# Performance work log

Hardware: AMD Instinct MI355X
Metric: run time of the kernel (lower is better)

Reference implementation:

```python
import jax, jax.numpy as jnp
import numpy as np

D = 20          # embedding dim (hardcoded in original module)
N_REL = 200     # relation vocab size (table has N_REL+1 rows)
N_TIME = 365    # time embedding table size
L = 3           # propagation layers
E = 2_000_000   # edges per layer
N = 1_000_000   # node-slot pool per layer
B = 64          # batch size
N_ENT = 1_000_003


def setup_inputs() -> dict:
    key = jax.random.key(0)
    ks = jax.random.split(key, 16)
    src_idx = jax.random.randint(ks[0], (L, E), 0, N, dtype=jnp.int32)
    dst_idx = jax.random.randint(ks[1], (L, E), 0, N, dtype=jnp.int32)
    rel_idx = jax.random.randint(ks[2], (L, E), 0, N_REL + 1, dtype=jnp.int32)
    qrel_idx = jax.random.randint(ks[3], (L, E), 0, N_REL + 1, dtype=jnp.int32)
    # signed relative time (edge_time - query_time); abs() must stay < N_TIME
    rel_time = jax.random.randint(ks[4], (L, E), -(N_TIME - 1), N_TIME, dtype=jnp.int32)
    node_batch = jax.random.randint(ks[5], (N,), 0, B, dtype=jnp.int32)
    node_ent = jnp.arange(N, dtype=jnp.int32)  # unique entity per final node slot
    s = 0.1
    rela_embed = jax.random.normal(ks[6], (N_REL + 1, D), jnp.float32) * s
    time_embed = jax.random.normal(ks[7], (N_TIME, D), jnp.float32) * s
    w_att1 = jax.random.normal(ks[8], (30, 3 * D), jnp.float32) * s
    w_att2 = jax.random.normal(ks[9], (1, 30), jnp.float32) * s
    w_past = jax.random.normal(ks[10], (D, D), jnp.float32) * s
    w_now = jax.random.normal(ks[11], (D, D), jnp.float32) * s
    w_future = jax.random.normal(ks[12], (D, D), jnp.float32) * s
    w_cls = jax.random.normal(ks[13], (D,), jnp.float32) * s
    b_cls = jnp.zeros((), jnp.float32)
    return dict(src_idx=src_idx, dst_idx=dst_idx, rel_idx=rel_idx,
                qrel_idx=qrel_idx, rel_time=rel_time, node_batch=node_batch,
                node_ent=node_ent, rela_embed=rela_embed, time_embed=time_embed,
                w_att1=w_att1, w_att2=w_att2, w_past=w_past, w_now=w_now,
                w_future=w_future, w_cls=w_cls, b_cls=b_cls,
                batch_size=B, n_ent=N_ENT)


def reference(src_idx, dst_idx, rel_idx, qrel_idx, rel_time, node_batch,
              node_ent, rela_embed, time_embed, w_att1, w_att2, w_past,
              w_now, w_future, w_cls, b_cls, batch_size, n_ent):
    n_layers = src_idx.shape[0]
    n_nodes = node_batch.shape[0]
    d = rela_embed.shape[1]
    hidden = jnp.zeros((n_nodes, d), dtype=rela_embed.dtype)
    for l in range(n_layers):
        rt = rel_time[l]                         # [E] signed relative time
        h_src = hidden[src_idx[l]]               # [E, D] gather
        r_emb = rela_embed[rel_idx[l]]           # [E, D]
        t_emb = time_embed[jnp.abs(rt)]          # [E, D]
        embed_rel = h_src + r_emb + t_emb
        # conditional time-branch MLP (mask-partitioned linear, same math as
        # the original's boolean-masked assignments)
        fut = embed_rel @ w_future.T
        now = embed_rel @ w_now.T
        pst = embed_rel @ w_past.T
        transformed = jnp.where((rt > 0)[:, None], fut,
                       jnp.where((rt == 0)[:, None], now, pst))
        # attention over concat(hidden_src, rel_emb, query_rel_emb)  [E, 3D]
        att_in = jnp.concatenate([h_src, r_emb, rela_embed[qrel_idx[l]]], axis=1)
        score = jax.nn.sigmoid(jax.nn.relu(att_in @ w_att1.T) @ w_att2.T)  # [E,1]
        msg = score * transformed                # [E, D]
        hidden = jax.ops.segment_sum(msg, dst_idx[l], num_segments=n_nodes)
        hidden = jax.nn.leaky_relu(hidden)       # default slope 0.01, as torch
    result = hidden @ w_cls + b_cls              # [N]
    score_all = jnp.zeros((batch_size, n_ent), dtype=result.dtype)
    score_all = score_all.at[node_batch, node_ent].set(result)
    return score_all
```

## Files before the change

### kernel.cpp

```cpp
#include <hip/hip_runtime.h>
#include <hip/hip_bf16.h>
#include <cstdint>

#define DD 20
#define HID 30
#define NB_SCAN 1024
#define MROW 21

__device__ __forceinline__ void load20(const float* __restrict__ p, float* r){
  const float4* q = (const float4*)p;
#pragma unroll
  for (int i=0;i<5;i++){ float4 v=q[i]; r[4*i+0]=v.x; r[4*i+1]=v.y; r[4*i+2]=v.z; r[4*i+3]=v.w; }
}

__global__ void k_prep(const float* __restrict__ rela, const float* __restrict__ w1,
                       const float* __restrict__ wp, const float* __restrict__ wn,
                       const float* __restrict__ wf,
                       float* __restrict__ W3, float* __restrict__ AR, float* __restrict__ AQ,
                       int nrel){
  int t = blockIdx.x*blockDim.x + threadIdx.x;
  if (t < 3*DD*DD){
    int s = t/(DD*DD), idx = t%(DD*DD);
    W3[t] = (s==0)?wp[idx]:((s==1)?wn[idx]:wf[idx]);
  }
  if (t < nrel*HID){
    int r=t/HID, j=t-r*HID;
    float sr=0.f, sq=0.f;
#pragma unroll
    for (int k=0;k<DD;k++){
      float e = rela[r*DD+k];
      sr += e*w1[j*3*DD + DD + k];
      sq += e*w1[j*3*DD + 2*DD + k];
    }
    AR[r*32+j]=sr; AQ[r*32+j]=sq;
  }
}

__global__ void k_rt(const float* __restrict__ rela, const float* __restrict__ timee,
                     const float* __restrict__ W3, float* __restrict__ RT,
                     int nrel, int ntime){
  int row = blockIdx.x*blockDim.x+threadIdx.x;
  int tot = 3*nrel*ntime;
  if (row>=tot) return;
  int per = nrel*ntime;
  int sel = row/per; int rem = row - sel*per; int r = rem/ntime; int t = rem - r*ntime;
  float e[DD], tv[DD];
  load20(rela + (size_t)r*DD, e);
  load20(timee + (size_t)t*DD, tv);
#pragma unroll
  for (int k=0;k<DD;k++) e[k]+=tv[k];
  const float* W = W3 + sel*DD*DD;
  float o[DD];
#pragma unroll
  for (int i=0;i<DD;i++){
    const float4* wr = (const float4*)(W + i*DD);
    float s=0.f;
#pragma unroll
    for (int c=0;c<5;c++){ float4 w=wr[c]; s += e[4*c]*w.x + e[4*c+1]*w.y + e[4*c+2]*w.z + e[4*c+3]*w.w; }
    o[i]=s;
  }
  float4* op=(float4*)(RT + (size_t)row*DD);
#pragma unroll
  for (int c=0;c<5;c++){ float4 v; v.x=o[4*c]; v.y=o[4*c+1]; v.z=o[4*c+2]; v.w=o[4*c+3]; op[c]=v; }
}

__global__ void __launch_bounds__(256) k_pre(const int* __restrict__ dst0, int* __restrict__ cnt0,
        int* __restrict__ rank0, int E,
        float4* __restrict__ dout4, size_t nd4,
        float4* __restrict__ b04, float4* __restrict__ b14, size_t nb4){
  int g=blockIdx.x, tid=threadIdx.x;
  int half=gridDim.x>>1;
  if (g & 1){
    int stride=half*256;
    for (int e=(g>>1)*256+tid; e<E; e+=stride)
      rank0[e]=atomicAdd(&cnt0[dst0[e]],1);
  } else {
    float4 z=make_float4(0.f,0.f,0.f,0.f);
    size_t i=(size_t)(g>>1)*256+tid, st=(size_t)half*256;
    for (size_t k=i;k<nd4;k+=st) dout4[k]=z;
    for (size_t k=i;k<nb4;k+=st){ b04[k]=z; b14[k]=z; }
  }
}

__global__ void k_scan_part(const int* __restrict__ cnt, int* __restrict__ part, int M, int C){
  __shared__ int sm[256];
  int b=blockIdx.x, t=threadIdx.x;
  int lo=b*C, hi=lo+C; if (hi>M) hi=M; if (lo>M) lo=M;
  int s=0;
  for (int i=lo+t; i<hi; i+=256) s+=cnt[i];
  sm[t]=s; __syncthreads();
  for (int o=128;o>0;o>>=1){ if (t<o) sm[t]+=sm[t+o]; __syncthreads(); }
  if (t==0) part[b]=sm[0];
}

__global__ void k_scan_top(int* __restrict__ part){
  __shared__ int sm[NB_SCAN];
  int t=threadIdx.x;
  int v=part[t]; sm[t]=v; __syncthreads();
  for (int o=1;o<NB_SCAN;o<<=1){
    int u=(t>=o)?sm[t-o]:0; __syncthreads();
    sm[t]+=u; __syncthreads();
  }
  part[t]=sm[t]-v;
}

__global__ void k_scan_write(const int* __restrict__ cnt, const int* __restrict__ part,
                             int* __restrict__ rowptr, int M, int C){
  __shared__ int sm[256];
  int b=blockIdx.x, t=threadIdx.x;
  int lo=b*C, hi=lo+C; if (hi>M) hi=M; if (lo>M) lo=M;
  int run=part[b];
  for (int base=lo; base<hi; base+=256){
    int i=base+t;
    int v=(i<hi)?cnt[i]:0;
    sm[t]=v; __syncthreads();
    for (int o=1;o<256;o<<=1){
      int u=(t>=o)?sm[t-o]:0; __syncthreads();
      sm[t]+=u; __syncthreads();
    }
    if (i<hi) rowptr[i]=run+sm[t]-v;
    int tot=sm[255];
    __syncthreads();
    run+=tot;
  }
  if (hi==M && t==0) rowptr[M]=run;
}

__global__ void __launch_bounds__(256) k_scat(const int* __restrict__ src,const int* __restrict__ dst,
  const int* __restrict__ rel,const int* __restrict__ qrel,const int* __restrict__ rtm,
  const int* __restrict__ rank,const int* __restrict__ rowptr,int4* __restrict__ recs,int E,
  int xb,int mode,
  float* __restrict__ dout,const int* __restrict__ nb,const int* __restrict__ ne,
  const int* __restrict__ nentp,const float* __restrict__ bcls,int N,
  float4* __restrict__ zbuf,size_t nz4,int* __restrict__ listc){
  int g=blockIdx.x, tid=threadIdx.x;
  if (g<xb){
    if (mode==0){
      float b=bcls[0]; long long stride=nentp[0];
      for (int n=g*256+tid;n<N;n+=xb*256) dout[(long long)nb[n]*stride+ne[n]]=b;
    } else {
      if (g==0&&tid==0) *listc=0;
      float4 z=make_float4(0.f,0.f,0.f,0.f);
      for (size_t k=(size_t)g*256+tid;k<nz4;k+=(size_t)xb*256) zbuf[k]=z;
    }
    return;
  }
  int e=(g-xb)*256+tid;
  if (e>=E) return;
  int d=dst[e];
  int pos=rowptr[d]+rank[e];
  recs[pos]=make_int4(src[e], rel[e]|(qrel[e]<<16), rtm[e], d);
}

template<bool HASH,bool HIST,bool FINAL>
__global__ void __launch_bounds__(256) k_fused(
    const int4* __restrict__ recs,
    const float* __restrict__ hin, float* __restrict__ hout,
    const float* __restrict__ RT, const float* __restrict__ AR, const float* __restrict__ AQ,
    const float* __restrict__ w1, const float* __restrict__ w2, const float* __restrict__ W3,
    int E, int nrel, int ntime,
    const int* __restrict__ ndst, int* __restrict__ ncnt, int* __restrict__ nrank, int nE,
    const float* __restrict__ wcls, const float* __restrict__ bcls,
    const int* __restrict__ nbv, const int* __restrict__ nev, const int* __restrict__ nentp,
    float* __restrict__ outp, int* __restrict__ list, int* __restrict__ listc)
{
  int lb;
  if (HIST){
    int g=blockIdx.x;
    int r=g%3, b3=g/3;
    if (r==2){
      int H=gridDim.x/3;
      int stride=H*256;
      for (int e=b3*256+threadIdx.x; e<nE; e+=stride)
        nrank[e]=atomicAdd(&ncnt[ndst[e]],1);
      return;
    }
    lb=b3*2+r;
  } else lb=blockIdx.x;
  int bstart=lb*256;
  if (bstart>=E) return;

  __shared__ float sW1h[HID*DD];
  __shared__ float sW2[32];
  __shared__ float sW3[3*DD*DD];
  __shared__ float smsg[256*MROW];
  __shared__ int   sdst[256];
  __shared__ int   s_prevdst, s_nextdst;
  if (HASH){
    for (int t=threadIdx.x; t<HID*DD; t+=blockDim.x){ int j=t/DD,k=t-j*DD; sW1h[t]=w1[j*3*DD+k]; }
    for (int t=threadIdx.x; t<3*DD*DD; t+=blockDim.x) sW3[t]=W3[t];
  }
  if (threadIdx.x<HID) sW2[threadIdx.x]=w2[threadIdx.x];

  int tid = threadIdx.x;
  int bsize = E - bstart; if (bsize>256) bsize=256;
  int j = bstart + tid;
  bool active = (tid < bsize);

  if (tid==0){
    s_prevdst = (bstart>0) ? recs[-1 + (ptrdiff_t)bstart].w : -1;
    s_nextdst = (bstart+bsize < E) ? recs[bstart+bsize].w : -1;
  }
  __syncthreads();

  int dstv = -1;
  float m[DD];
  if (active){
    int4 rc = recs[j];
    int s = rc.x;
    int r = rc.y & 0xFFFF;
    int q = ((unsigned)rc.y) >> 16;
    int t = rc.z;
    dstv  = rc.w;
    int sel = (t>0)?2:((t==0)?1:0);
    int ta = (t<0)?-t:t;

    float h[DD];
    if (HASH){
      load20(hin+(size_t)s*DD, h);
#pragma unroll
      for (int i=0;i<DD;i++) h[i]=fmaxf(h[i],0.01f*h[i]);
    }

    float a[HID];
    {
      const float4* ap=(const float4*)(AR+(size_t)r*32);
      const float4* qp=(const float4*)(AQ+(size_t)q*32);
#pragma unroll
      for (int c=0;c<7;c++){
        float4 x=ap[c], y=qp[c];
        a[4*c+0]=x.x+y.x; a[4*c+1]=x.y+y.y; a[4*c+2]=x.z+y.z; a[4*c+3]=x.w+y.w;
      }
      float2 x=*(const float2*)(AR+(size_t)r*32+28);
      float2 y=*(const float2*)(AQ+(size_t)q*32+28);
      a[28]=x.x+y.x; a[29]=x.y+y.y;
    }
    if (HASH){
#pragma unroll
      for (int jj=0;jj<HID;jj++){
        const float4* wr=(const float4*)&sW1h[jj*DD];
        float sum=a[jj];
#pragma unroll
        for (int c=0;c<5;c++){ float4 w=wr[c]; sum += h[4*c]*w.x+h[4*c+1]*w.y+h[4*c+2]*w.z+h[4*c+3]*w.w; }
        a[jj]=sum;
      }
    }
    float z=0.f;
#pragma unroll
    for (int jj=0;jj<HID;jj++) z += fmaxf(a[jj],0.f)*sW2[jj];
    float score = 1.f/(1.f+__expf(-z));

    float tr[DD];
    load20(RT + ((size_t)(sel*nrel+r)*ntime + ta)*DD, tr);
    if (HASH){
      const float* Ws = sW3 + sel*DD*DD;
#pragma unroll
      for (int i=0;i<DD;i++){
        const float4* wr=(const float4*)(Ws+i*DD);
        float sum=tr[i];
#pragma unroll
        for (int c=0;c<5;c++){ float4 w=wr[c]; sum += h[4*c]*w.x+h[4*c+1]*w.y+h[4*c+2]*w.z+h[4*c+3]*w.w; }
        tr[i]=sum;
      }
    }
#pragma unroll
    for (int i=0;i<DD;i++){ m[i]=score*tr[i]; smsg[tid*MROW+i]=m[i]; }
  }
  sdst[tid] = active ? dstv : -2;
  __syncthreads();

  if (!active) return;
  bool isHead = (tid==0) ? (s_prevdst != dstv) : (sdst[tid-1] != dstv);
  if (!(isHead || tid==0)) return;
  int k=tid+1;
  for (; k<bsize && sdst[k]==dstv; ++k){
    const float* row=&smsg[k*MROW];
#pragma unroll
    for (int i=0;i<DD;i++) m[i]+=row[i];
  }
  bool crossStart = (tid==0 && !isHead);
  bool crossEnd   = (k==bsize) && (s_nextdst==dstv);
  if (crossStart || crossEnd){
    float* o = hout + (size_t)dstv*DD;
#pragma unroll
    for (int i=0;i<DD;i++) atomicAdd(o+i, m[i]);
    if (FINAL && isHead){
      int p = atomicAdd(listc,1);
      list[p] = dstv;
    }
  } else {
    if (!FINAL){
      float4* op=(float4*)(hout + (size_t)dstv*DD);
#pragma unroll
      for (int c=0;c<5;c++){ float4 v; v.x=m[4*c]; v.y=m[4*c+1]; v.z=m[4*c+2]; v.w=m[4*c+3]; op[c]=v; }
    } else {
      float rsum=bcls[0];
#pragma unroll
      for (int i=0;i<DD;i++){ float x=fmaxf(m[i],0.01f*m[i]); rsum += x*wcls[i]; }
      long long stride = nentp[0];
      outp[(long long)nbv[dstv]*stride + nev[dstv]] = rsum;
    }
  }
}

__global__ void __launch_bounds__(256) k_fsparse(const float* __restrict__ buf,
   const float* __restrict__ wcls,const float* __restrict__ bcls,
   const int* __restrict__ nb,const int* __restrict__ ne,const int* __restrict__ nentp,
   float* __restrict__ out,const int* __restrict__ list,const int* __restrict__ listc){
  int c=*listc;
  int i=blockIdx.x*blockDim.x+threadIdx.x;
  if (i>=c) return;
  int n=list[i];
  float rsum=bcls[0];
  const float* h=buf+(size_t)n*DD;
#pragma unroll
  for (int jj=0;jj<DD;jj++){ float v=h[jj]; float x=fmaxf(v,0.01f*v); rsum+=x*wcls[jj]; }
  long long stride=nentp[0];
  out[(long long)nb[n]*stride+ne[n]]=rsum;
}

template<bool HASH>
__global__ void __launch_bounds__(256) k_edge(
    const int* __restrict__ src, const int* __restrict__ dst,
    const int* __restrict__ rel, const int* __restrict__ qrel,
    const int* __restrict__ rtm,
    const float* __restrict__ hin, float* __restrict__ hout,
    const float* __restrict__ RT, const float* __restrict__ AR, const float* __restrict__ AQ,
    const float* __restrict__ w1, const float* __restrict__ w2, const float* __restrict__ W3,
    int E, int nrel, int ntime)
{
  __shared__ float sW1h[HID*DD];
  __shared__ float sW2[32];
  __shared__ float sW3[3*DD*DD];
  for (int t=threadIdx.x; t<HID*DD; t+=blockDim.x){ int j=t/DD,k=t-j*DD; sW1h[t]=w1[j*3*DD+k]; }
  if (threadIdx.x<HID) sW2[threadIdx.x]=w2[threadIdx.x];
  for (int t=threadIdx.x; t<3*DD*DD; t+=blockDim.x) sW3[t]=W3[t];
  __syncthreads();
  int e = blockIdx.x*blockDim.x+threadIdx.x;
  if (e>=E) return;
  int s=src[e], d=dst[e], r=rel[e], q=qrel[e], t=rtm[e];
  int sel = (t>0)?2:((t==0)?1:0);
  int ta = (t<0)?-t:t;
  float h[DD];
  if (HASH){
    load20(hin+(size_t)s*DD, h);
#pragma unroll
    for (int i=0;i<DD;i++) h[i]=fmaxf(h[i],0.01f*h[i]);
  }
  float a[HID];
  {
    const float4* ap=(const float4*)(AR+(size_t)r*32);
    const float4* qp=(const float4*)(AQ+(size_t)q*32);
#pragma unroll
    for (int c=0;c<7;c++){
      float4 x=ap[c], y=qp[c];
      a[4*c+0]=x.x+y.x; a[4*c+1]=x.y+y.y; a[4*c+2]=x.z+y.z; a[4*c+3]=x.w+y.w;
    }
    float2 x=*(const float2*)(AR+(size_t)r*32+28);
    float2 y=*(const float2*)(AQ+(size_t)q*32+28);
    a[28]=x.x+y.x; a[29]=x.y+y.y;
  }
  if (HASH){
#pragma unroll
    for (int j=0;j<HID;j++){
      const float4* wr=(const float4*)&sW1h[j*DD];
      float sum=a[j];
#pragma unroll
      for (int c=0;c<5;c++){ float4 w=wr[c]; sum += h[4*c]*w.x+h[4*c+1]*w.y+h[4*c+2]*w.z+h[4*c+3]*w.w; }
      a[j]=sum;
    }
  }
  float z=0.f;
#pragma unroll
  for (int j=0;j<HID;j++) z += fmaxf(a[j],0.f)*sW2[j];
  float score = 1.f/(1.f+__expf(-z));
  float tr[DD];
  load20(RT + ((size_t)(sel*nrel+r)*ntime + ta)*DD, tr);
  if (HASH){
    const float* Ws = sW3 + sel*DD*DD;
#pragma unroll
    for (int i=0;i<DD;i++){
      const float4* wr=(const float4*)(Ws+i*DD);
      float sum=tr[i];
#pragma unroll
      for (int c=0;c<5;c++){ float4 w=wr[c]; sum += h[4*c]*w.x+h[4*c+1]*w.y+h[4*c+2]*w.z+h[4*c+3]*w.w; }
      tr[i]=sum;
    }
  }
  float* o = hout + (size_t)d*DD;
#pragma unroll
  for (int i=0;i<DD;i++) atomicAdd(o+i, score*tr[i]);
}

__global__ void k_result(const float* __restrict__ h, const float* __restrict__ wcls,
                         const float* __restrict__ bcls, float* __restrict__ res, int N){
  int i = blockIdx.x*blockDim.x+threadIdx.x;
  if (i>=N) return;
  float acc = bcls[0];
  const float4* q=(const float4*)(h+(size_t)i*DD);
#pragma unroll
  for (int c=0;c<5;c++){
    float4 v=q[c];
    float x0=fmaxf(v.x,0.01f*v.x), x1=fmaxf(v.y,0.01f*v.y);
    float x2=fmaxf(v.z,0.01f*v.z), x3=fmaxf(v.w,0.01f*v.w);
    acc += x0*wcls[4*c]+x1*wcls[4*c+1]+x2*wcls[4*c+2]+x3*wcls[4*c+3];
  }
  res[i]=acc;
}

__global__ void k_scatter(const float* __restrict__ res, const int* __restrict__ nb,
                          const int* __restrict__ ne, const int* __restrict__ nentp,
                          float* __restrict__ out, int N){
  int i=blockIdx.x*blockDim.x+threadIdx.x;
  if (i>=N) return;
  long long stride = nentp[0];
  out[(long long)nb[i]*stride + ne[i]] = res[i];
}

extern "C" void kernel_launch(void* const* d_in, const int* in_sizes, int n_in,
                              void* d_out, int out_size, void* d_ws, size_t ws_size,
                              hipStream_t stream){
  const int*   src =(const int*)d_in[0];
  const int*   dst =(const int*)d_in[1];
  const int*   rel =(const int*)d_in[2];
  const int*   qrel=(const int*)d_in[3];
  const int*   rtm =(const int*)d_in[4];
  const int*   nb  =(const int*)d_in[5];
  const int*   ne  =(const int*)d_in[6];
  const float* rela=(const float*)d_in[7];
  const float* timee=(const float*)d_in[8];
  const float* w1  =(const float*)d_in[9];
  const float* w2  =(const float*)d_in[10];
  const float* wp  =(const float*)d_in[11];
  const float* wn  =(const float*)d_in[12];
  const float* wf  =(const float*)d_in[13];
  const float* wcls=(const float*)d_in[14];
  const float* bcls=(const float*)d_in[15];
  const int*   nentp=(const int*)d_in[17];

  const int Lc=3;
  int LE=in_sizes[0]; int E=LE/Lc;
  int N=in_sizes[5];
  int nrel=in_sizes[7]/DD;
  int ntime=in_sizes[8]/DD;

  auto al=[](size_t x){ return (x+(size_t)255)&~(size_t)255; };
  size_t szBuf =al((size_t)N*DD*4);
  size_t szRT  =al((size_t)3*nrel*ntime*DD*4);
  size_t szA   =al((size_t)nrel*32*4);
  size_t szW3  =al((size_t)3*DD*DD*4);
  size_t szRow =al((size_t)Lc*((size_t)N+1)*4);
  size_t szRank=al((size_t)LE*4);
  size_t szCnt =al((size_t)Lc*N*4);
  size_t szRecs=al((size_t)LE*16);
  size_t szPart=al((size_t)NB_SCAN*4);
  size_t szList=al((size_t)(8192+16)*4);
  size_t need = 2*szBuf+szRT+2*szA+szW3+szRow+szRank+szCnt+szRecs+szPart+szList;

  dim3 blk(256);
  int prepTot = (3*DD*DD > nrel*HID) ? 3*DD*DD : nrel*HID;
  int rtTot=3*nrel*ntime;

  if (ws_size >= need){
    char* base=(char*)d_ws;
    size_t off=0;
    float* buf0=(float*)(base+off); off+=szBuf;
    float* buf1=(float*)(base+off); off+=szBuf;
    float* RT  =(float*)(base+off); off+=szRT;
    float* AR  =(float*)(base+off); off+=szA;
    float* AQ  =(float*)(base+off); off+=szA;
    float* W3  =(float*)(base+off); off+=szW3;
    int*   rowptr=(int*)(base+off); off+=szRow;
    int*   rank=(int*)(base+off);  off+=szRank;
    int*   cnt =(int*)(base+off);  off+=szCnt;
    int4*  recs=(int4*)(base+off); off+=szRecs;
    int*   part=(int*)(base+off);  off+=szPart;
    int*   listc=(int*)(base+off);
    int*   list =listc+16;          off+=szList;

    float* dout=(float*)d_out;

    (void)hipMemsetAsync(cnt,0,(size_t)Lc*N*4,stream);
    k_prep<<<dim3((prepTot+255)/256),blk,0,stream>>>(rela,w1,wp,wn,wf,W3,AR,AQ,nrel);
    k_rt<<<dim3((rtTot+255)/256),blk,0,stream>>>(rela,timee,W3,RT,nrel,ntime);

    size_t nd4=(size_t)out_size>>2;
    size_t nb4=(size_t)N*DD/4;
    k_pre<<<dim3(8192),blk,0,stream>>>(dst,cnt,rank,E,(float4*)dout,nd4,(float4*)buf0,(float4*)buf1,nb4);

    int C=(N+NB_SCAN-1)/NB_SCAN;
    int LB=(E+255)/256;
    int H=(LB+1)/2;

    for (int l=0;l<Lc;++l){
      int* cnt_l = cnt + (size_t)l*N;
      int* row_l = rowptr + (size_t)l*(N+1);
      k_scan_part<<<dim3(NB_SCAN),blk,0,stream>>>(cnt_l,part,N,C);
      k_scan_top<<<dim3(1),dim3(NB_SCAN),0,stream>>>(part);
      k_scan_write<<<dim3(NB_SCAN),blk,0,stream>>>(cnt_l,part,row_l,N,C);
      size_t eo=(size_t)l*E;
      int xb = (l==0)?1024:((l==2)?2048:0);
      int mode=(l==0)?0:2;
      k_scat<<<dim3(xb+LB),blk,0,stream>>>(src+eo,dst+eo,rel+eo,qrel+eo,rtm+eo,
          rank+eo,row_l,recs+eo,E,xb,mode,
          dout,nb,ne,nentp,bcls,N,(float4*)buf0,nb4,listc);
      if (l==0){
        k_fused<false,true,false><<<dim3(3*H),blk,0,stream>>>(recs,nullptr,buf0,
            RT,AR,AQ,w1,w2,W3,E,nrel,ntime,
            dst+(size_t)E,cnt+(size_t)N,rank+(size_t)E,E,
            nullptr,nullptr,nullptr,nullptr,nullptr,nullptr,nullptr,nullptr);
      } else if (l==1){
        k_fused<true,true,false><<<dim3(3*H),blk,0,stream>>>(recs+(size_t)E,buf0,buf1,
            RT,AR,AQ,w1,w2,W3,E,nrel,ntime,
            dst+(size_t)2*E,cnt+(size_t)2*N,rank+(size_t)2*E,E,
            nullptr,nullptr,nullptr,nullptr,nullptr,nullptr,nullptr,nullptr);
      } else {
        k_fused<true,false,true><<<dim3(LB),blk,0,stream>>>(recs+(size_t)2*E,buf1,buf0,
            RT,AR,AQ,w1,w2,W3,E,nrel,ntime,
            nullptr,nullptr,nullptr,0,
            wcls,bcls,nb,ne,nentp,dout,list,listc);
      }
    }
    k_fsparse<<<dim3(32),blk,0,stream>>>(buf0,wcls,bcls,nb,ne,nentp,dout,list,listc);
  } else {
    char* base=(char*)d_out; float* res=(float*)d_ws;
    size_t off=0;
    float* buf0=(float*)(base+off); off+=szBuf;
    float* buf1=(float*)(base+off); off+=szBuf;
    float* RT  =(float*)(base+off); off+=szRT;
    float* AR  =(float*)(base+off); off+=szA;
    float* AQ  =(float*)(base+off); off+=szA;
    float* W3  =(float*)(base+off); off+=szW3;
    k_prep<<<dim3((prepTot+255)/256),blk,0,stream>>>(rela,w1,wp,wn,wf,W3,AR,AQ,nrel);
    k_rt<<<dim3((rtTot+255)/256),blk,0,stream>>>(rela,timee,W3,RT,nrel,ntime);
    dim3 egrid((E+255)/256);
    dim3 ngrid((N+255)/256);
    (void)hipMemsetAsync(buf0,0,(size_t)N*DD*4,stream);
    k_edge<false><<<egrid,blk,0,stream>>>(src,dst,rel,qrel,rtm,nullptr,buf0,RT,AR,AQ,w1,w2,W3,E,nrel,ntime);
    (void)hipMemsetAsync(buf1,0,(size_t)N*DD*4,stream);
    k_edge<true><<<egrid,blk,0,stream>>>(src+(size_t)E,dst+(size_t)E,rel+(size_t)E,qrel+(size_t)E,rtm+(size_t)E,
                                         buf0,buf1,RT,AR,AQ,w1,w2,W3,E,nrel,ntime);
    (void)hipMemsetAsync(buf0,0,(size_t)N*DD*4,stream);
    k_edge<true><<<egrid,blk,0,stream>>>(src+(size_t)2*E,dst+(size_t)2*E,rel+(size_t)2*E,qrel+(size_t)2*E,rtm+(size_t)2*E,
                                         buf1,buf0,RT,AR,AQ,w1,w2,W3,E,nrel,ntime);
    k_result<<<ngrid,blk,0,stream>>>(buf0,wcls,bcls,res,N);
    (void)hipMemsetAsync(d_out,0,(size_t)out_size*sizeof(float),stream);
    k_scatter<<<ngrid,blk,0,stream>>>(res,nb,ne,nentp,(float*)d_out,N);
  }
}
```

Before: 1.122 ms.

## Store intermediate hidden states in bf16 with per-layer atomic fixup buffer

Hidden node states between layers are now stored as bf16 in 64-byte padded rows, with leaky_relu applied before packing, which halves gather traffic for the per-edge source lookups. Segments that cross block boundaries accumulate into a separate fp32 buffer via atomics, and their node ids are appended to a list. A per-layer fixup kernel then applies the activation, packs those nodes to bf16 and clears the fp32 rows. This adds two small kernel launches and bf16 rounding error in exchange for less memory bandwidth.

Measured after the change: 1.134 ms. About the same (+1.0%).

```diff
diff --git a/kernel.cpp b/kernel.cpp
--- a/kernel.cpp
+++ b/kernel.cpp
@@ -6,11 +6,21 @@
 #define HID 30
 #define NB_SCAN 1024
 #define MROW 21
+#define HROW 32
+
+typedef unsigned int  u32;
+typedef unsigned short u16;
 
 __device__ __forceinline__ void load20(const float* __restrict__ p, float* r){
   const float4* q = (const float4*)p;
 #pragma unroll
   for (int i=0;i<5;i++){ float4 v=q[i]; r[4*i+0]=v.x; r[4*i+1]=v.y; r[4*i+2]=v.z; r[4*i+3]=v.w; }
+}
+
+__device__ __forceinline__ u32 pkbf(float a, float b){
+  u32 ua=__float_as_uint(a); ua=(ua+0x7FFFu+((ua>>16)&1u))>>16;
+  u32 ub=__float_as_uint(b); ub=(ub+0x7FFFu+((ub>>16)&1u))>>16;
+  return ua | (ub<<16);
 }
 
 __global__ void k_prep(const float* __restrict__ rela, const float* __restrict__ w1,
@@ -67,7 +77,8 @@
 __global__ void __launch_bounds__(256) k_pre(const int* __restrict__ dst0, int* __restrict__ cnt0,
         int* __restrict__ rank0, int E,
         float4* __restrict__ dout4, size_t nd4,
-        float4* __restrict__ b04, float4* __restrict__ b14, size_t nb4){
+        uint4* __restrict__ b0, uint4* __restrict__ b1, size_t nbB4,
+        float4* __restrict__ bF, size_t nf4){
   int g=blockIdx.x, tid=threadIdx.x;
   int half=gridDim.x>>1;
   if (g & 1){
@@ -76,9 +87,11 @@
       rank0[e]=atomicAdd(&cnt0[dst0[e]],1);
   } else {
     float4 z=make_float4(0.f,0.f,0.f,0.f);
+    uint4 zu=make_uint4(0u,0u,0u,0u);
     size_t i=(size_t)(g>>1)*256+tid, st=(size_t)half*256;
     for (size_t k=i;k<nd4;k+=st) dout4[k]=z;
-    for (size_t k=i;k<nb4;k+=st){ b04[k]=z; b14[k]=z; }
+    for (size_t k=i;k<nbB4;k+=st){ b0[k]=zu; b1[k]=zu; }
+    for (size_t k=i;k<nf4;k+=st) bF[k]=z;
   }
 }
 
@@ -93,9 +106,10 @@
   if (t==0) part[b]=sm[0];
 }
 
-__global__ void k_scan_top(int* __restrict__ part){
+__global__ void k_scan_top(int* __restrict__ part, int* __restrict__ listc){
   __shared__ int sm[NB_SCAN];
   int t=threadIdx.x;
+  if (t==0) *listc=0;
   int v=part[t]; sm[t]=v; __syncthreads();
   for (int o=1;o<NB_SCAN;o<<=1){
     int u=(t>=o)?sm[t-o]:0; __syncthreads();
@@ -129,20 +143,13 @@
 __global__ void __launch_bounds__(256) k_scat(const int* __restrict__ src,const int* __restrict__ dst,
   const int* __restrict__ rel,const int* __restrict__ qrel,const int* __restrict__ rtm,
   const int* __restrict__ rank,const int* __restrict__ rowptr,int4* __restrict__ recs,int E,
-  int xb,int mode,
+  int xb,
   float* __restrict__ dout,const int* __restrict__ nb,const int* __restrict__ ne,
-  const int* __restrict__ nentp,const float* __restrict__ bcls,int N,
-  float4* __restrict__ zbuf,size_t nz4,int* __restrict__ listc){
+  const int* __restrict__ nentp,const float* __restrict__ bcls,int N){
   int g=blockIdx.x, tid=threadIdx.x;
   if (g<xb){
-    if (mode==0){
-      float b=bcls[0]; long long stride=nentp[0];
-      for (int n=g*256+tid;n<N;n+=xb*256) dout[(long long)nb[n]*stride+ne[n]]=b;
-    } else {
-      if (g==0&&tid==0) *listc=0;
-      float4 z=make_float4(0.f,0.f,0.f,0.f);
-      for (size_t k=(size_t)g*256+tid;k<nz4;k+=(size_t)xb*256) zbuf[k]=z;
-    }
+    float b=bcls[0]; long long stride=nentp[0];
+    for (int n=g*256+tid;n<N;n+=xb*256) dout[(long long)nb[n]*stride+ne[n]]=b;
     return;
   }
   int e=(g-xb)*256+tid;
@@ -155,7 +162,7 @@
 template<bool HASH,bool HIST,bool FINAL>
 __global__ void __launch_bounds__(256) k_fused(
     const int4* __restrict__ recs,
-    const float* __restrict__ hin, float* __restrict__ hout,
+    const u16* __restrict__ hin, u16* __restrict__ hout, float* __restrict__ bufF,
     const float* __restrict__ RT, const float* __restrict__ AR, const float* __restrict__ AQ,
     const float* __restrict__ w1, const float* __restrict__ w2, const float* __restrict__ W3,
     int E, int nrel, int ntime,
@@ -217,9 +224,14 @@
 
     float h[DD];
     if (HASH){
-      load20(hin+(size_t)s*DD, h);
-#pragma unroll
-      for (int i=0;i<DD;i++) h[i]=fmaxf(h[i],0.01f*h[i]);
+      const uint4* hp=(const uint4*)(hin+(size_t)s*HROW);
+      uint4 A=hp[0], B=hp[1]; uint2 Cc=*((const uint2*)(hp+2));
+      u32 w10[10]={A.x,A.y,A.z,A.w,B.x,B.y,B.z,B.w,Cc.x,Cc.y};
+#pragma unroll
+      for (int i2=0;i2<10;i2++){
+        h[2*i2]  =__uint_as_float(w10[i2]<<16);
+        h[2*i2+1]=__uint_as_float(w10[i2]&0xFFFF0000u);
+      }
     }
 
     float a[HID];
@@ -281,18 +293,26 @@
   bool crossStart = (tid==0 && !isHead);
   bool crossEnd   = (k==bsize) && (s_nextdst==dstv);
   if (crossStart || crossEnd){
-    float* o = hout + (size_t)dstv*DD;
+    float* o = bufF + (size_t)dstv*DD;
 #pragma unroll
     for (int i=0;i<DD;i++) atomicAdd(o+i, m[i]);
-    if (FINAL && isHead){
+    if (isHead){
       int p = atomicAdd(listc,1);
       list[p] = dstv;
     }
   } else {
     if (!FINAL){
-      float4* op=(float4*)(hout + (size_t)dstv*DD);
-#pragma unroll
-      for (int c=0;c<5;c++){ float4 v; v.x=m[4*c]; v.y=m[4*c+1]; v.z=m[4*c+2]; v.w=m[4*c+3]; op[c]=v; }
+      u32 o10[10];
+#pragma unroll
+      for (int i2=0;i2<10;i2++){
+        float x0=m[2*i2], x1=m[2*i2+1];
+        x0=fmaxf(x0,0.01f*x0); x1=fmaxf(x1,0.01f*x1);
+        o10[i2]=pkbf(x0,x1);
+      }
+      uint4* hp=(uint4*)(hout+(size_t)dstv*HROW);
+      hp[0]=make_uint4(o10[0],o10[1],o10[2],o10[3]);
+      hp[1]=make_uint4(o10[4],o10[5],o10[6],o10[7]);
+      *((uint2*)(hp+2))=make_uint2(o10[8],o10[9]);
     } else {
       float rsum=bcls[0];
 #pragma unroll
@@ -303,7 +323,8 @@
   }
 }
 
-__global__ void __launch_bounds__(256) k_fsparse(const float* __restrict__ buf,
+template<bool FINAL>
+__global__ void __launch_bounds__(256) k_fixup(float* __restrict__ bufF, u16* __restrict__ hout,
    const float* __restrict__ wcls,const float* __restrict__ bcls,
    const int* __restrict__ nb,const int* __restrict__ ne,const int* __restrict__ nentp,
    float* __restrict__ out,const int* __restrict__ list,const int* __restrict__ listc){
@@ -311,12 +332,29 @@
   int i=blockIdx.x*blockDim.x+threadIdx.x;
   if (i>=c) return;
   int n=list[i];
-  float rsum=bcls[0];
-  const float* h=buf+(size_t)n*DD;
-#pragma unroll
-  for (int jj=0;jj<DD;jj++){ float v=h[jj]; float x=fmaxf(v,0.01f*v); rsum+=x*wcls[jj]; }
-  long long stride=nentp[0];
-  out[(long long)nb[n]*stride+ne[n]]=rsum;
+  float* p=bufF+(size_t)n*DD;
+  float v[DD];
+#pragma unroll
+  for (int jj=0;jj<DD;jj++){ v[jj]=p[jj]; p[jj]=0.f; }
+  if (FINAL){
+    float rsum=bcls[0];
+#pragma unroll
+    for (int jj=0;jj<DD;jj++){ float x=fmaxf(v[jj],0.01f*v[jj]); rsum+=x*wcls[jj]; }
+    long long stride=nentp[0];
+    out[(long long)nb[n]*stride+ne[n]]=rsum;
+  } else {
+    u32 o10[10];
+#pragma unroll
+    for (int i2=0;i2<10;i2++){
+      float x0=v[2*i2], x1=v[2*i2+1];
+      x0=fmaxf(x0,0.01f*x0); x1=fmaxf(x1,0.01f*x1);
+      o10[i2]=pkbf(x0,x1);
+    }
+    uint4* hp=(uint4*)(hout+(size_t)n*HROW);
+    hp[0]=make_uint4(o10[0],o10[1],o10[2],o10[3]);
+    hp[1]=make_uint4(o10[4],o10[5],o10[6],o10[7]);
+    *((uint2*)(hp+2))=make_uint2(o10[8],o10[9]);
+  }
 }
 
 template<bool HASH>
@@ -445,6 +483,8 @@
   int ntime=in_sizes[8]/DD;
 
   auto al=[](size_t x){ return (x+(size_t)255)&~(size_t)255; };
+  size_t szBufB=al((size_t)N*HROW*2);
+  size_t szBufF=al((size_t)N*DD*4);
   size_t szBuf =al((size_t)N*DD*4);
   size_t szRT  =al((size_t)3*nrel*ntime*DD*4);
   size_t szA   =al((size_t)nrel*32*4);
@@ -454,8 +494,8 @@
   size_t szCnt =al((size_t)Lc*N*4);
   size_t szRecs=al((size_t)LE*16);
   size_t szPart=al((size_t)NB_SCAN*4);
-  size_t szList=al((size_t)(8192+16)*4);
-  size_t need = 2*szBuf+szRT+2*szA+szW3+szRow+szRank+szCnt+szRecs+szPart+szList;
+  size_t szList=al((size_t)(32768+16)*4);
+  size_t need = 2*szBufB+szBufF+szRT+2*szA+szW3+szRow+szRank+szCnt+szRecs+szPart+szList;
 
   dim3 blk(256);
   int prepTot = (3*DD*DD > nrel*HID) ? 3*DD*DD : nrel*HID;
@@ -464,8 +504,9 @@
   if (ws_size >= need){
     char* base=(char*)d_ws;
     size_t off=0;
-    float* buf0=(float*)(base+off); off+=szBuf;
-    float* buf1=(float*)(base+off); off+=szBuf;
+    u16*   b0 =(u16*)(base+off);   off+=szBufB;
+    u16*   b1 =(u16*)(base+off);   off+=szBufB;
+    float* bufF=(float*)(base+off); off+=szBufF;
     float* RT  =(float*)(base+off); off+=szRT;
     float* AR  =(float*)(base+off); off+=szA;
     float* AQ  =(float*)(base+off); off+=szA;
@@ -485,8 +526,10 @@
     k_rt<<<dim3((rtTot+255)/256),blk,0,stream>>>(rela,timee,W3,RT,nrel,ntime);
 
     size_t nd4=(size_t)out_size>>2;
-    size_t nb4=(size_t)N*DD/4;
-    k_pre<<<dim3(8192),blk,0,stream>>>(dst,cnt,rank,E,(float4*)dout,nd4,(float4*)buf0,(float4*)buf1,nb4);
+    size_t nbB4=(size_t)N*HROW*2/16;
+    size_t nf4=(size_t)N*DD/4;
+    k_pre<<<dim3(8192),blk,0,stream>>>(dst,cnt,rank,E,(float4*)dout,nd4,
+                                       (uint4*)b0,(uint4*)b1,nbB4,(float4*)bufF,nf4);
 
     int C=(N+NB_SCAN-1)/NB_SCAN;
     int LB=(E+255)/256;
@@ -496,32 +539,32 @@
       int* cnt_l = cnt + (size_t)l*N;
       int* row_l = rowptr + (size_t)l*(N+1);
       k_scan_part<<<dim3(NB_SCAN),blk,0,stream>>>(cnt_l,part,N,C);
-      k_scan_top<<<dim3(1),dim3(NB_SCAN),0,stream>>>(part);
+      k_scan_top<<<dim3(1),dim3(NB_SCAN),0,stream>>>(part,listc);
       k_scan_write<<<dim3(NB_SCAN),blk,0,stream>>>(cnt_l,part,row_l,N,C);
       size_t eo=(size_t)l*E;
-      int xb = (l==0)?1024:((l==2)?2048:0);
-      int mode=(l==0)?0:2;
+      int xb = (l==0)?1024:0;
       k_scat<<<dim3(xb+LB),blk,0,stream>>>(src+eo,dst+eo,rel+eo,qrel+eo,rtm+eo,
-          rank+eo,row_l,recs+eo,E,xb,mode,
-          dout,nb,ne,nentp,bcls,N,(float4*)buf0,nb4,listc);
+          rank+eo,row_l,recs+eo,E,xb,dout,nb,ne,nentp,bcls,N);
       if (l==0){
-        k_fused<false,true,false><<<dim3(3*H),blk,0,stream>>>(recs,nullptr,buf0,
+        k_fused<false,true,false><<<dim3(3*H),blk,0,stream>>>(recs,nullptr,b0,bufF,
             RT,AR,AQ,w1,w2,W3,E,nrel,ntime,
             dst+(size_t)E,cnt+(size_t)N,rank+(size_t)E,E,
-            nullptr,nullptr,nullptr,nullptr,nullptr,nullptr,nullptr,nullptr);
+            nullptr,nullptr,nullptr,nullptr,nullptr,nullptr,list,listc);
+        k_fixup<false><<<dim3(128),blk,0,stream>>>(bufF,b0,wcls,bcls,nb,ne,nentp,dout,list,listc);
       } else if (l==1){
-        k_fused<true,true,false><<<dim3(3*H),blk,0,stream>>>(recs+(size_t)E,buf0,buf1,
+        k_fused<true,true,false><<<dim3(3*H),blk,0,stream>>>(recs+(size_t)E,b0,b1,bufF,
             RT,AR,AQ,w1,w2,W3,E,nrel,ntime,
             dst+(size_t)2*E,cnt+(size_t)2*N,rank+(size_t)2*E,E,
-            nullptr,nullptr,nullptr,nullptr,nullptr,nullptr,nullptr,nullptr);
+            nullptr,nullptr,nullptr,nullptr,nullptr,nullptr,list,listc);
+        k_fixup<false><<<dim3(128),blk,0,stream>>>(bufF,b1,wcls,bcls,nb,ne,nentp,dout,list,listc);
       } else {
-        k_fused<true,false,true><<<dim3(LB),blk,0,stream>>>(recs+(size_t)2*E,buf1,buf0,
+        k_fused<true,false,true><<<dim3(LB),blk,0,stream>>>(recs+(size_t)2*E,b1,nullptr,bufF,
             RT,AR,AQ,w1,w2,W3,E,nrel,ntime,
             nullptr,nullptr,nullptr,0,
             wcls,bcls,nb,ne,nentp,dout,list,listc);
+        k_fixup<true><<<dim3(128),blk,0,stream>>>(bufF,nullptr,wcls,bcls,nb,ne,nentp,dout,list,listc);
       }
     }
-    k_fsparse<<<dim3(32),blk,0,stream>>>(buf0,wcls,bcls,nb,ne,nentp,dout,list,listc);
   } else {
     char* base=(char*)d_out; float* res=(float*)d_ws;
     size_t off=0;
```
